# Performance work log

Hardware: AMD Instinct MI355X
Metric: run time of the kernel (lower is better)

The kernel has to match this reference:

```python
import jax, jax.numpy as jnp
import numpy as np

_SHAPE = (4, 2, 8, 256, 513)  # N, 2(real/imag), C, T, F


def setup_inputs() -> dict:
    key = jax.random.key(0)
    k1, k2, k3 = jax.random.split(key, 3)
    return {
        "mixture": jax.random.normal(k1, _SHAPE, dtype=jnp.float32),
        "target": jax.random.normal(k2, _SHAPE, dtype=jnp.float32),
        "noise": jax.random.normal(k3, _SHAPE, dtype=jnp.float32),
        "ref_mic_idx": 0,
    }


def _to_complex(x):
    # (N, 2, C, T, F) real-imag stacked -> complex (N, C, T, F)
    return jax.lax.complex(x[:, 0], x[:, 1])


def _mean_spatial_cov(s):
    # s: complex (N, C, T, F) -> time-averaged covariance (N, F, C, C)
    N, C, T, F = s.shape
    sc = jnp.transpose(s, (0, 3, 2, 1))  # (N, F, T, C)
    # outer product V V^H summed over T, fused into one batched GEMM
    return jnp.einsum("nftc,nftd->nfcd", sc, jnp.conj(sc)) / T


def reference(mixture, target, noise, ref_mic_idx):
    y = _to_complex(mixture)  # (N, C, T, F)
    x = _to_complex(target)
    v = _to_complex(noise)
    N, C, T, F = y.shape

    phi_target = _mean_spatial_cov(x)  # (N, F, C, C)
    # diagonal loading: torch adds load to BOTH real and imag parts (RI dim broadcast)
    load = (0.001 / np.sqrt(2)) * (1.0 + 1.0j)
    phi_noise = _mean_spatial_cov(v) + jnp.asarray(load, dtype=y.dtype) * jnp.eye(C, dtype=y.dtype)

    G = jnp.linalg.inv(phi_noise) @ phi_target  # (N, F, C, C)
    l = jnp.trace(G, axis1=-2, axis2=-1)  # (N, F)
    # W = (1/l) * G @ e_ref  -> select column ref_mic_idx
    W = G[..., ref_mic_idx] / l[..., None]  # (N, F, C)

    # X_bf(n,t,f) = W^H y = sum_c conj(W)_{nfc} y_{nctf}
    X_bf = jnp.einsum("nfc,nctf->ntf", jnp.conj(W), y)  # (N, T, F)
    # restack real/imag and add singleton channel dim -> (N, 2, 1, T, F)
    out = jnp.stack([X_bf.real, X_bf.imag], axis=1)[:, :, None]
    return out
```

## Files before the change

### kernel.cpp

```cpp
#include <hip/hip_runtime.h>

#define Nn 4
#define Cc 8
#define Tt 256
#define Ff 513
#define TFs (Tt * Ff)
#define NPAIR 36
#define NCHUNK 32
#define TCHUNK (Tt / NCHUNK)

#define COV_BYTES ((size_t)2 * Nn * 72 * Ff * 4)

template <int G>
__device__ __forceinline__ void cov_body(const float* __restrict__ base,
                                         float* __restrict__ dst, int t0)
{
    constexpr int R2 = 7 - G;
    float ar[9], ai[9];
#pragma unroll
    for (int s = 0; s < 9; ++s) { ar[s] = 0.f; ai[s] = 0.f; }

    const float* bt = base + (size_t)t0 * Ff;
#pragma unroll
    for (int tt = 0; tt < TCHUNK; ++tt) {
        float re[8], im[8];
#pragma unroll
        for (int c = G; c < 8; ++c) {
            re[c] = bt[(size_t)c * TFs];
            im[c] = bt[(size_t)(Cc + c) * TFs];
        }
        int s = 0;
#pragma unroll
        for (int d = G; d < 8; ++d, ++s) {
            ar[s] += re[G] * re[d] + im[G] * im[d];
            ai[s] += im[G] * re[d] - re[G] * im[d];
        }
#pragma unroll
        for (int d = R2; d < 8; ++d, ++s) {
            ar[s] += re[R2] * re[d] + im[R2] * im[d];
            ai[s] += im[R2] * re[d] - re[R2] * im[d];
        }
        bt += Ff;
    }

    int s = 0;
#pragma unroll
    for (int d = G; d < 8; ++d, ++s) {
        const int p = G * 8 - G * (G - 1) / 2 + (d - G);
        atomicAdd(dst + (size_t)(p * 2 + 0) * Ff, ar[s]);
        atomicAdd(dst + (size_t)(p * 2 + 1) * Ff, ai[s]);
    }
#pragma unroll
    for (int d = R2; d < 8; ++d, ++s) {
        const int p = R2 * 8 - R2 * (R2 - 1) / 2 + (d - R2);
        atomicAdd(dst + (size_t)(p * 2 + 0) * Ff, ar[s]);
        atomicAdd(dst + (size_t)(p * 2 + 1) * Ff, ai[s]);
    }
}

__global__ __launch_bounds__(64) void cov_accum(
    const float* __restrict__ target, const float* __restrict__ noise,
    float* __restrict__ covbuf)
{
    int f = blockIdx.x * 64 + threadIdx.x;
    if (f >= Ff) return;
    int n = blockIdx.y;
    int z = blockIdx.z;
    int g = z & 3;
    int inp = (z >> 2) & 1;
    int chunk = z >> 3;

    const float* src = inp ? noise : target;
    const float* base = src + (size_t)n * 2 * Cc * TFs + f;
    float* dst = covbuf + ((size_t)(inp * Nn + n) * 72) * Ff + f;
    int t0 = chunk * TCHUNK;

    switch (g) {
        case 0: cov_body<0>(base, dst, t0); break;
        case 1: cov_body<1>(base, dst, t0); break;
        case 2: cov_body<2>(base, dst, t0); break;
        default: cov_body<3>(base, dst, t0); break;
    }
}

__global__ __launch_bounds__(256) void mvdr_weights(
    const float* __restrict__ covbuf, const int* __restrict__ ref_ptr,
    float2* __restrict__ wconj)
{
    const int tid = threadIdx.x;
    const int n = blockIdx.y;
    const int fbase = blockIdx.x * 16;

    __shared__ float cov[16][144];

    {
        int f_off = tid & 15;
        int vrow = tid >> 4;
        int f = fbase + f_off;
#pragma unroll
        for (int b = 0; b < 9; ++b) {
            int v = b * 16 + vrow;
            int inp = v >= 72 ? 1 : 0;
            int p2 = v - 72 * inp;
            float val = 0.f;
            if (f < Ff)
                val = covbuf[((size_t)(inp * Nn + n) * 72 + p2) * Ff + f];
            cov[f_off][v] = val;
        }
    }
    __syncthreads();

    const int prob = tid >> 4;
    const int col = tid & 15;
    const int f = fbase + prob;

    const float invT = 1.0f / (float)Tt;
    const float dl = 0.001f / 1.41421356237309515f;

    float Ar[8], Ai[8];
    {
        const bool left = (col < 8);
        const int c = left ? col : col - 8;
        const float* cv = &cov[prob][left ? 72 : 0];
#pragma unroll
        for (int r = 0; r < 8; ++r) {
            int lo = r <= c ? r : c, hi = r <= c ? c : r;
            int p = lo * 8 - lo * (lo - 1) / 2 + (hi - lo);
            float vr = cv[2 * p] * invT;
            float vi = cv[2 * p + 1] * invT;
            if (r > c) vi = -vi;
            if (left && r == c) { vr += dl; vi += dl; }
            Ar[r] = vr; Ai[r] = vi;
        }
    }

#pragma unroll
    for (int k = 0; k < 8; ++k) {
        int best = k;
        float bm = Ar[k] * Ar[k] + Ai[k] * Ai[k];
#pragma unroll
        for (int j = 0; j < 8; ++j) {
            if (j > k) {
                float m = Ar[j] * Ar[j] + Ai[j] * Ai[j];
                if (m > bm) { bm = m; best = j; }
            }
        }
        int bk = __shfl(best, k, 16);

        float tr = Ar[k], ti = Ai[k];
#pragma unroll
        for (int j = 0; j < 8; ++j) {
            if (j == bk && j != k) {
                Ar[k] = Ar[j]; Ai[k] = Ai[j];
                Ar[j] = tr;    Ai[j] = ti;
            }
        }

        float pr = __shfl(Ar[k], k, 16);
        float pi = __shfl(Ai[k], k, 16);
        float d = pr * pr + pi * pi;
        float ir = pr / d, ii = -pi / d;
        float nr = Ar[k] * ir - Ai[k] * ii;
        float ni = Ar[k] * ii + Ai[k] * ir;
        Ar[k] = nr; Ai[k] = ni;

#pragma unroll
        for (int r = 0; r < 8; ++r) {
            float fr = __shfl(Ar[r], k, 16);
            float fi = __shfl(Ai[r], k, 16);
            if (r != k) {
                Ar[r] -= fr * Ar[k] - fi * Ai[k];
                Ai[r] -= fr * Ai[k] + fi * Ar[k];
            }
        }
    }

    float tlr = 0.f, tli = 0.f;
    if (col >= 8) { tlr = Ar[col - 8]; tli = Ai[col - 8]; }
#pragma unroll
    for (int off = 1; off < 16; off <<= 1) {
        tlr += __shfl_xor(tlr, off, 16);
        tli += __shfl_xor(tli, off, 16);
    }

    int ref = *ref_ptr;
    if (col == 8 + ref && f < Ff) {
        float den = tlr * tlr + tli * tli;
        float2* wp = wconj + ((size_t)n * Ff + f) * 8;
#pragma unroll
        for (int r = 0; r < 8; ++r) {
            float wx = (Ar[r] * tlr + Ai[r] * tli) / den;
            float wy = (Ai[r] * tlr - Ar[r] * tli) / den;
            wp[r] = make_float2(wx, -wy);
        }
    }
}

__global__ __launch_bounds__(256) void beamform(
    const float* __restrict__ y, const float2* __restrict__ wconj,
    float* __restrict__ out)
{
    int idx = blockIdx.x * 256 + threadIdx.x;
    int n = idx / (TFs / 2);
    int m = (idx - n * (TFs / 2)) * 2;
    int f0 = m % Ff;
    int f1 = (f0 + 1 == Ff) ? 0 : f0 + 1;

    const float2* yb = (const float2*)y + ((size_t)n * 2 * Cc * TFs + m) / 2;
    const float2* w0 = wconj + ((size_t)n * Ff + f0) * 8;
    const float2* w1 = wconj + ((size_t)n * Ff + f1) * 8;

    float xr0 = 0.f, xi0 = 0.f, xr1 = 0.f, xi1 = 0.f;
#pragma unroll
    for (int c = 0; c < Cc; ++c) {
        float2 yre = yb[(size_t)c * (TFs / 2)];
        float2 yim = yb[(size_t)(Cc + c) * (TFs / 2)];
        float2 a = w0[c], b = w1[c];
        xr0 += a.x * yre.x - a.y * yim.x;
        xi0 += a.x * yim.x + a.y * yre.x;
        xr1 += b.x * yre.y - b.y * yim.y;
        xi1 += b.x * yim.y + b.y * yre.y;
    }
    size_t ob = ((size_t)n * 2 * TFs + m) / 2;
    ((float2*)out)[ob] = make_float2(xr0, xr1);
    ((float2*)out)[ob + TFs / 2] = make_float2(xi0, xi1);
}

extern "C" void kernel_launch(void* const* d_in, const int* in_sizes, int n_in,
                              void* d_out, int out_size, void* d_ws, size_t ws_size,
                              hipStream_t stream) {
    const float* mixture = (const float*)d_in[0];
    const float* target  = (const float*)d_in[1];
    const float* noise   = (const float*)d_in[2];
    const int*   refp    = (const int*)d_in[3];
    float* out = (float*)d_out;

    float*  covbuf = (float*)d_ws;
    float2* wconj  = (float2*)((char*)d_ws + COV_BYTES);

    hipMemsetAsync(d_ws, 0, COV_BYTES, stream);

    cov_accum<<<dim3(9, Nn, NCHUNK * 8), 64, 0, stream>>>(target, noise, covbuf);
    mvdr_weights<<<dim3((Ff + 15) / 16, Nn), 256, 0, stream>>>(covbuf, refp, wconj);
    beamform<<<dim3((Nn * TFs / 2) / 256), 256, 0, stream>>>(mixture, wconj, out);
}
```

Before: 175.3 us.

## Replace atomic covariance accumulation with per-chunk partials reduced in weights kernel

Covariance accumulation now writes per-time-chunk partial sums to a workspace buffer with plain stores instead of atomicAdd. The mvdr_weights kernel sums the partials while loading them, which also removes the memset launch. The time-chunk count is halved to limit partial-buffer size. The cost is more workspace traffic (about 19 MB written then read), a serial reduction loop in the weights kernel, and fewer blocks in the covariance pass.

```diff
diff --git a/kernel.cpp b/kernel.cpp
--- a/kernel.cpp
+++ b/kernel.cpp
@@ -6,10 +6,11 @@
 #define Ff 513
 #define TFs (Tt * Ff)
 #define NPAIR 36
-#define NCHUNK 32
+#define NCHUNK 16
 #define TCHUNK (Tt / NCHUNK)
 
-#define COV_BYTES ((size_t)2 * Nn * 72 * Ff * 4)
+#define PARTIAL_FLOATS ((size_t)2 * Nn * NCHUNK * 72 * Ff)
+#define PARTIAL_BYTES  (PARTIAL_FLOATS * 4)
 
 template <int G>
 __device__ __forceinline__ void cov_body(const float* __restrict__ base,
@@ -47,20 +48,20 @@
 #pragma unroll
     for (int d = G; d < 8; ++d, ++s) {
         const int p = G * 8 - G * (G - 1) / 2 + (d - G);
-        atomicAdd(dst + (size_t)(p * 2 + 0) * Ff, ar[s]);
-        atomicAdd(dst + (size_t)(p * 2 + 1) * Ff, ai[s]);
+        dst[(size_t)(p * 2 + 0) * Ff] = ar[s];
+        dst[(size_t)(p * 2 + 1) * Ff] = ai[s];
     }
 #pragma unroll
     for (int d = R2; d < 8; ++d, ++s) {
         const int p = R2 * 8 - R2 * (R2 - 1) / 2 + (d - R2);
-        atomicAdd(dst + (size_t)(p * 2 + 0) * Ff, ar[s]);
-        atomicAdd(dst + (size_t)(p * 2 + 1) * Ff, ai[s]);
-    }
-}
-
-__global__ __launch_bounds__(64) void cov_accum(
+        dst[(size_t)(p * 2 + 0) * Ff] = ar[s];
+        dst[(size_t)(p * 2 + 1) * Ff] = ai[s];
+    }
+}
+
+__global__ __launch_bounds__(64) void cov_partial(
     const float* __restrict__ target, const float* __restrict__ noise,
-    float* __restrict__ covbuf)
+    float* __restrict__ partial)
 {
     int f = blockIdx.x * 64 + threadIdx.x;
     if (f >= Ff) return;
@@ -72,7 +73,8 @@
 
     const float* src = inp ? noise : target;
     const float* base = src + (size_t)n * 2 * Cc * TFs + f;
-    float* dst = covbuf + ((size_t)(inp * Nn + n) * 72) * Ff + f;
+    float* dst = partial +
+        (((size_t)(inp * Nn + n) * NCHUNK + chunk) * 72) * Ff + f;
     int t0 = chunk * TCHUNK;
 
     switch (g) {
@@ -84,7 +86,7 @@
 }
 
 __global__ __launch_bounds__(256) void mvdr_weights(
-    const float* __restrict__ covbuf, const int* __restrict__ ref_ptr,
+    const float* __restrict__ partial, const int* __restrict__ ref_ptr,
     float2* __restrict__ wconj)
 {
     const int tid = threadIdx.x;
@@ -102,10 +104,15 @@
             int v = b * 16 + vrow;
             int inp = v >= 72 ? 1 : 0;
             int p2 = v - 72 * inp;
-            float val = 0.f;
-            if (f < Ff)
-                val = covbuf[((size_t)(inp * Nn + n) * 72 + p2) * Ff + f];
-            cov[f_off][v] = val;
+            float acc = 0.f;
+            if (f < Ff) {
+                const float* src = partial +
+                    ((size_t)(inp * Nn + n) * NCHUNK * 72 + p2) * Ff + f;
+#pragma unroll
+                for (int ch = 0; ch < NCHUNK; ++ch)
+                    acc += src[(size_t)ch * 72 * Ff];
+            }
+            cov[f_off][v] = acc;
         }
     }
     __syncthreads();
@@ -235,12 +242,12 @@
     const int*   refp    = (const int*)d_in[3];
     float* out = (float*)d_out;
 
-    float*  covbuf = (float*)d_ws;
-    float2* wconj  = (float2*)((char*)d_ws + COV_BYTES);
-
-    hipMemsetAsync(d_ws, 0, COV_BYTES, stream);
-
-    cov_accum<<<dim3(9, Nn, NCHUNK * 8), 64, 0, stream>>>(target, noise, covbuf);
-    mvdr_weights<<<dim3((Ff + 15) / 16, Nn), 256, 0, stream>>>(covbuf, refp, wconj);
+    float*  partial = (float*)d_ws;
+    float2* wconj   = (float2*)((char*)d_ws + PARTIAL_BYTES);
+
+    cov_partial<<<dim3(9, Nn, NCHUNK * 8), 64, 0, stream>>>(
+        target, noise, partial);
+    mvdr_weights<<<dim3((Ff + 15) / 16, Nn), 256, 0, stream>>>(
+        partial, refp, wconj);
     beamform<<<dim3((Nn * TFs / 2) / 256), 256, 0, stream>>>(mixture, wconj, out);
 }
```

New measurement: 167.5 us. 1.05x faster.
